# Kernel tuning notes

Hardware: AMD Instinct MI355X
Metric: run time of the kernel (lower is better)

## Reference

```python
import jax, jax.numpy as jnp
import numpy as np

B, S, D, E, H = 8, 1024, 1024, 8, 4096  # batch, seq, n_embd, num_experts, 4*n_embd


def setup_inputs() -> dict:
    key = jax.random.key(0)
    ks = jax.random.split(key, 8)
    sc = 0.02
    return {
        "x": jax.random.normal(ks[0], (B, S, D), jnp.float32),
        "noise": jax.random.normal(ks[1], (B, S, E), jnp.float32),
        "Wg": jax.random.normal(ks[2], (D, E), jnp.float32) * sc,
        "bg": jnp.zeros((E,), jnp.float32),
        "Wn": jax.random.normal(ks[3], (D, E), jnp.float32) * sc,
        "bn": jnp.zeros((E,), jnp.float32),
        "W1": jax.random.normal(ks[4], (E, D, H), jnp.float32) * sc,
        "b1": jnp.zeros((E, H), jnp.float32),
        "W2": jax.random.normal(ks[5], (E, H, D), jnp.float32) * sc,
        "b2": jnp.zeros((E, D), jnp.float32),
        "top_k": 2,
    }


def reference(x, noise, Wg, bg, Wn, bn, W1, b1, W2, b2, top_k):
    # --- NoisyTopkRouter ---
    logits = jnp.einsum("bsd,de->bse", x, Wg) + bg
    noise_logits = jnp.einsum("bsd,de->bse", x, Wn) + bn
    noisy = logits + noise * jax.nn.softplus(noise_logits)  # [B,S,E]
    _, idx = jax.lax.top_k(noisy, top_k)  # [B,S,K]
    in_topk = jax.nn.one_hot(idx, noisy.shape[-1], dtype=noisy.dtype).sum(-2) > 0
    sparse_logits = jnp.where(in_topk, noisy, -jnp.inf)
    gating = jax.nn.softmax(sparse_logits, axis=-1)  # zero outside top-k

    # --- dispatch/combine: gating is exactly zero for non-selected experts,
    # so per-expert masked gather + weighted scatter-add == gated dense sum ---
    g_e = jnp.moveaxis(gating, -1, 0)  # [E,B,S]

    def body(acc, params):
        W1e, b1e, W2e, b2e, ge = params
        h = jax.nn.relu(jnp.einsum("bsd,dh->bsh", x, W1e) + b1e)  # [B,S,H]
        y = (jnp.einsum("bsh,hd->bsd", h, W2e) + b2e) * ge[..., None]
        return acc + y, y

    final_output, expert_outputs = jax.lax.scan(
        body, jnp.zeros_like(x), (W1, b1, W2, b2, g_e)
    )
    # expert_outputs: [E,B,S,D], matching the per-expert weighted outputs list
    return final_output, expert_outputs, gating
```

## Files before the change

### kernel.cpp

```cpp
#include <hip/hip_runtime.h>
#include <hip/hip_bf16.h>
#include <stdint.h>

#define TKN   8192
#define DD    1024
#define EE    8
#define HH    4096
#define TOPK  2
#define NASG  (TKN * TOPK)
#define NSLOT 72

typedef unsigned short u16;
typedef __bf16 bf16x8 __attribute__((ext_vector_type(8)));
typedef float  f32x4  __attribute__((ext_vector_type(4)));

__device__ __forceinline__ u16 f2bf(float f) {
  __hip_bfloat16 h = __float2bfloat16(f);
  return __builtin_bit_cast(u16, h);
}
__device__ __forceinline__ float bf2f(u16 u) {
  uint32_t v = ((uint32_t)u) << 16;
  return __builtin_bit_cast(float, v);
}

__device__ __forceinline__ void glds16(const void* g, void* l) {
  __builtin_amdgcn_global_load_lds(
      (__attribute__((address_space(1))) void*)g,
      (__attribute__((address_space(3))) void*)l, 16, 0, 0);
}

#define FENCE() asm volatile("" ::: "memory")
#define BAR()   do { FENCE(); __builtin_amdgcn_s_barrier(); FENCE(); } while (0)
#define VMCNT0() asm volatile("s_waitcnt vmcnt(0)" ::: "memory")

__global__ __launch_bounds__(256) void transpose_cvt_kernel(
    const float* __restrict__ src, u16* __restrict__ dst, int R, int C) {
  __shared__ float tile[64][33];
  int e = blockIdx.z;
  int c0 = blockIdx.x * 32, r0 = blockIdx.y * 64;
  int tx = threadIdx.x, ty = threadIdx.y;
  const float* s = src + (size_t)e * R * C;
  uint32_t* d32 = (uint32_t*)(dst + (size_t)e * R * C);
#pragma unroll
  for (int j = 0; j < 8; j++)
    tile[ty * 8 + j][tx] = s[(size_t)(r0 + ty * 8 + j) * C + c0 + tx];
  __syncthreads();
#pragma unroll
  for (int jj = 0; jj < 4; jj++) {
    int c = c0 + ty * 4 + jj;
    uint32_t lo = f2bf(tile[2 * tx][ty * 4 + jj]);
    uint32_t hi = f2bf(tile[2 * tx + 1][ty * 4 + jj]);
    d32[((size_t)c * R + r0) / 2 + tx] = lo | (hi << 16);
  }
}

__global__ __launch_bounds__(256) void router_kernel(
    const float* __restrict__ x, const float* __restrict__ noise,
    const float* __restrict__ Wg, const float* __restrict__ bg,
    const float* __restrict__ Wn, const float* __restrict__ bn,
    float* __restrict__ gating, u16* __restrict__ xb,
    int* __restrict__ sel_e, float* __restrict__ sel_g) {
  int t = blockIdx.x;
  int tid = threadIdx.x;
  float acc[16];
#pragma unroll
  for (int j = 0; j < 16; j++) acc[j] = 0.f;
  for (int i = tid; i < DD; i += 256) {
    float xv = x[(size_t)t * DD + i];
    xb[(size_t)t * DD + i] = f2bf(xv);
    const float4* g4 = (const float4*)(Wg + (size_t)i * EE);
    const float4* n4 = (const float4*)(Wn + (size_t)i * EE);
    float4 ga = g4[0], gb = g4[1];
    float4 na = n4[0], nb = n4[1];
    acc[0] += xv * ga.x;  acc[1] += xv * ga.y;  acc[2] += xv * ga.z;  acc[3] += xv * ga.w;
    acc[4] += xv * gb.x;  acc[5] += xv * gb.y;  acc[6] += xv * gb.z;  acc[7] += xv * gb.w;
    acc[8] += xv * na.x;  acc[9] += xv * na.y;  acc[10] += xv * na.z; acc[11] += xv * na.w;
    acc[12] += xv * nb.x; acc[13] += xv * nb.y; acc[14] += xv * nb.z; acc[15] += xv * nb.w;
  }
  __shared__ float red[4][16];
  int lane = tid & 63, wv = tid >> 6;
#pragma unroll
  for (int j = 0; j < 16; j++) {
    float v = acc[j];
    for (int o = 32; o > 0; o >>= 1) v += __shfl_down(v, o);
    acc[j] = v;
  }
  if (lane == 0) {
#pragma unroll
    for (int j = 0; j < 16; j++) red[wv][j] = acc[j];
  }
  __syncthreads();
  if (tid == 0) {
    float nz[EE];
#pragma unroll
    for (int e = 0; e < EE; e++) {
      float dg = red[0][e] + red[1][e] + red[2][e] + red[3][e] + bg[e];
      float dn = red[0][8 + e] + red[1][8 + e] + red[2][8 + e] + red[3][8 + e] + bn[e];
      float sp = fmaxf(dn, 0.f) + log1pf(expf(-fabsf(dn)));
      nz[e] = dg + noise[(size_t)t * EE + e] * sp;
    }
    int m1 = 0;
    for (int e = 1; e < EE; e++) if (nz[e] > nz[m1]) m1 = e;
    int m2 = (m1 == 0) ? 1 : 0;
    for (int e = 0; e < EE; e++) if (e != m1 && nz[e] > nz[m2]) m2 = e;
    float eb = expf(nz[m2] - nz[m1]);
    float den = 1.f + eb;
    float g1 = 1.f / den, g2 = eb / den;
    gating[(size_t)t * EE + m1] = g1;
    gating[(size_t)t * EE + m2] = g2;
    sel_e[t * 2] = m1; sel_e[t * 2 + 1] = m2;
    sel_g[t * 2] = g1; sel_g[t * 2 + 1] = g2;
  }
}

__global__ __launch_bounds__(256) void hist_scan_kernel(
    const int* __restrict__ sel_e, int* __restrict__ counts,
    int* __restrict__ offsets, int* __restrict__ cursors,
    int* __restrict__ slots) {
  __shared__ int hist[EE];
  int tid = threadIdx.x;
  if (tid < EE) hist[tid] = 0;
  __syncthreads();
  for (int i = tid; i < NASG; i += 256) atomicAdd(&hist[sel_e[i]], 1);
  __syncthreads();
  if (tid == 0) {
    int off = 0, ns = 0;
    for (int e = 0; e < EE; e++) {
      int c = hist[e];
      counts[e] = c; offsets[e] = off; cursors[e] = off; off += c;
      int nrt = (c + 255) >> 8;
      for (int rt = 0; rt < nrt; rt++) slots[ns++] = (e << 16) | rt;
    }
    for (; ns < NSLOT; ns++) slots[ns] = -1;
  }
}

__global__ __launch_bounds__(256) void build_lists_kernel(
    const int* __restrict__ sel_e, const float* __restrict__ sel_g,
    int* __restrict__ cursors, int* __restrict__ tok_list,
    float* __restrict__ gate_list, int* __restrict__ asg_of) {
  int t = blockIdx.x * 256 + threadIdx.x;
  int lane = threadIdx.x & 63;
#pragma unroll
  for (int k = 0; k < TOPK; k++) {
    int e = sel_e[t * 2 + k];
    float g = sel_g[t * 2 + k];
    for (int ee = 0; ee < EE; ee++) {
      unsigned long long m = __ballot(e == ee);
      if (m) {
        int leader = __ffsll(m) - 1;
        int base = 0;
        if (lane == leader) base = atomicAdd(&cursors[ee], __popcll(m));
        base = __shfl(base, leader);
        if (e == ee) {
          int slot = base + __popcll(m & ((1ull << lane) - 1ull));
          tok_list[slot] = t;
          gate_list[slot] = g;
          asg_of[t * 2 + k] = slot;
        }
      }
    }
  }
}

__global__ __launch_bounds__(256) void zerofill_kernel(
    const float* __restrict__ gating, float* __restrict__ expert_out) {
  int id = blockIdx.x;
  int e = id >> 13, t = id & (TKN - 1);
  if (gating[(size_t)t * EE + e] != 0.f) return;
  float4* p = (float4*)(expert_out + ((size_t)e * TKN + t) * DD);
  p[threadIdx.x] = (float4){0.f, 0.f, 0.f, 0.f};
}

__global__ __launch_bounds__(256) void combine_kernel(
    const float* __restrict__ expert_out, const int* __restrict__ sel_e,
    float* __restrict__ final_out) {
  int t = blockIdx.x;
  int e1 = sel_e[2 * t], e2 = sel_e[2 * t + 1];
  const float4* r1 = (const float4*)(expert_out + ((size_t)e1 * TKN + t) * DD);
  const float4* r2 = (const float4*)(expert_out + ((size_t)e2 * TKN + t) * DD);
  float4* o = (float4*)(final_out + (size_t)t * DD);
  int i = threadIdx.x;
  float4 a = r1[i], b = r2[i];
  o[i] = (float4){a.x + b.x, a.y + b.y, a.z + b.z, a.w + b.w};
}

__global__ __launch_bounds__(256) void merge_combine_kernel(
    const u16* __restrict__ part, const int* __restrict__ asg_of,
    const int* __restrict__ sel_e, const float* __restrict__ sel_g,
    const float* __restrict__ b2, float* __restrict__ expert_out,
    float* __restrict__ final_out) {
  int t = blockIdx.x;
  int i = threadIdx.x;
  int i1 = asg_of[2 * t], i2 = asg_of[2 * t + 1];
  int e1 = sel_e[2 * t], e2 = sel_e[2 * t + 1];
  float g1 = sel_g[2 * t], g2 = sel_g[2 * t + 1];
  float s1[4] = {0.f, 0.f, 0.f, 0.f}, s2[4] = {0.f, 0.f, 0.f, 0.f};
#pragma unroll
  for (int kq = 0; kq < 4; kq++) {
    ushort4 a = ((const ushort4*)(part + ((size_t)kq * NASG + i1) * DD))[i];
    ushort4 b = ((const ushort4*)(part + ((size_t)kq * NASG + i2) * DD))[i];
    s1[0] += bf2f(a.x); s1[1] += bf2f(a.y); s1[2] += bf2f(a.z); s1[3] += bf2f(a.w);
    s2[0] += bf2f(b.x); s2[1] += bf2f(b.y); s2[2] += bf2f(b.z); s2[3] += bf2f(b.w);
  }
  float4 bb1 = ((const float4*)(b2 + (size_t)e1 * DD))[i];
  float4 bb2 = ((const float4*)(b2 + (size_t)e2 * DD))[i];
  float4 y1 = {(s1[0] + bb1.x) * g1, (s1[1] + bb1.y) * g1,
               (s1[2] + bb1.z) * g1, (s1[3] + bb1.w) * g1};
  float4 y2 = {(s2[0] + bb2.x) * g2, (s2[1] + bb2.y) * g2,
               (s2[2] + bb2.z) * g2, (s2[3] + bb2.w) * g2};
  ((float4*)(expert_out + ((size_t)e1 * TKN + t) * DD))[i] = y1;
  ((float4*)(expert_out + ((size_t)e2 * TKN + t) * DD))[i] = y2;
  ((float4*)(final_out + (size_t)t * DD))[i] =
      (float4){y1.x + y2.x, y1.y + y2.y, y1.z + y2.z, y1.w + y2.w};
}

template<int KLOOP, int KSTRIDE, bool GATHER, int EPI, int LOGC>
__global__ __launch_bounds__(512, 2) void gemm8_kernel(
    const u16* __restrict__ A, const u16* __restrict__ Bm,
    const float* __restrict__ bias, const int* __restrict__ tok_list,
    const float* __restrict__ gate_list, const int* __restrict__ counts,
    const int* __restrict__ offsets, const int* __restrict__ slots,
    int Ncols, u16* __restrict__ OutBf, float* __restrict__ outF,
    u16* __restrict__ outP) {
  constexpr int NT = KLOOP / 64;
  int gid = blockIdx.x;
  int q = gid >> 3;
  constexpr int PERX = 9 << LOGC;
  int kq = q / PERX;
  int r0q = q - kq * PERX;
  int slot = (gid & 7) * 9 + (r0q >> LOGC);
  int ct = r0q & ((1 << LOGC) - 1);
  int packed = slots[slot];
  if (packed < 0) return;
  int e = packed >> 16;
  int rt = packed & 0xffff;
  int cnt = counts[e];
  int off = offsets[e];
  int col0 = ct * 256;
  int k0e = kq * KLOOP;

  __shared__ __attribute__((aligned(16))) char ldsc[131072];

  int tid = threadIdx.x;
  int w = tid >> 6, l = tid & 63;
  int wm = w >> 2, wn = w & 3;
  int fr = l & 15, hi = l >> 4;
  int kk16 = hi << 4;
  int xr = (fr & 7) << 4;

  int rl0 = w * 8 + (l >> 3);
  int slotE = ((l & 7) ^ ((l >> 3) & 7)) << 3;
  const u16* aptr[4];
  const u16* bptr[4];
#pragma unroll
  for (int i = 0; i < 4; i++) {
    int r = rt * 256 + rl0 + i * 64;
    if (GATHER) {
      int idx = min(off + r, NASG - 1);
      aptr[i] = A + (size_t)tok_list[idx] * KSTRIDE + k0e + slotE;
    } else {
      aptr[i] = A + (size_t)(off + r) * KSTRIDE + k0e + slotE;
    }
    bptr[i] = Bm + ((size_t)e * Ncols + col0 + rl0 + i * 64) * KSTRIDE + k0e + slotE;
  }
  char* ldsA = ldsc;
  char* ldsB = ldsc + 65536;

  auto issueAB = [&](int t) {
    char* db = ldsB + (t & 1) * 32768 + w * 1024;
    char* da = ldsA + (t & 1) * 32768 + w * 1024;
    glds16(bptr[0] + t * 64, db);
    glds16(bptr[1] + t * 64, db + 8192);
    glds16(bptr[2] + t * 64, db + 16384);
    glds16(bptr[3] + t * 64, db + 24576);
    glds16(aptr[0] + t * 64, da);
    glds16(aptr[1] + t * 64, da + 8192);
    glds16(aptr[2] + t * 64, da + 16384);
    glds16(aptr[3] + t * 64, da + 24576);
  };

  f32x4 acc[8][4];
#pragma unroll
  for (int m = 0; m < 8; m++)
#pragma unroll
    for (int n = 0; n < 4; n++) acc[m][n] = (f32x4){0.f, 0.f, 0.f, 0.f};
  bf16x8 aF[4][2], bF0[2][2], bF1[2][2];

  issueAB(0);
  VMCNT0();
  BAR();

  for (int t = 0; t < NT; t++) {
    int abase = (t & 1) * 32768;
    int bbase = 65536 + (t & 1) * 32768;
    if (t + 1 < NT) issueAB(t + 1);
#pragma unroll
    for (int mm = 0; mm < 4; mm++)
#pragma unroll
      for (int ks = 0; ks < 2; ks++)
        aF[mm][ks] = *(const bf16x8*)(ldsc + abase + (wm * 128 + mm * 16 + fr) * 128 +
                                      ((ks * 64 + kk16) ^ xr));
#pragma unroll
    for (int nn = 0; nn < 2; nn++)
#pragma unroll
      for (int ks = 0; ks < 2; ks++) {
        bF0[nn][ks] = *(const bf16x8*)(ldsc + bbase + (wn * 64 + nn * 16 + fr) * 128 +
                                       ((ks * 64 + kk16) ^ xr));
        bF1[nn][ks] = *(const bf16x8*)(ldsc + bbase + (wn * 64 + 32 + nn * 16 + fr) * 128 +
                                       ((ks * 64 + kk16) ^ xr));
      }
    __builtin_amdgcn_s_setprio(1);
#pragma unroll
    for (int mm = 0; mm < 4; mm++) {
#pragma unroll
      for (int nn = 0; nn < 2; nn++)
#pragma unroll
        for (int ks = 0; ks < 2; ks++) {
          acc[mm][nn]     = __builtin_amdgcn_mfma_f32_16x16x32_bf16(aF[mm][ks], bF0[nn][ks], acc[mm][nn], 0, 0, 0);
          acc[mm][2 + nn] = __builtin_amdgcn_mfma_f32_16x16x32_bf16(aF[mm][ks], bF1[nn][ks], acc[mm][2 + nn], 0, 0, 0);
        }
      __builtin_amdgcn_sched_barrier(0);
#pragma unroll
      for (int ks = 0; ks < 2; ks++)
        aF[mm][ks] = *(const bf16x8*)(ldsc + abase + (wm * 128 + 64 + mm * 16 + fr) * 128 +
                                      ((ks * 64 + kk16) ^ xr));
      __builtin_amdgcn_sched_barrier(0);
    }
#pragma unroll
    for (int mm = 0; mm < 4; mm++)
#pragma unroll
      for (int nn = 0; nn < 2; nn++)
#pragma unroll
        for (int ks = 0; ks < 2; ks++) {
          acc[4 + mm][nn]     = __builtin_amdgcn_mfma_f32_16x16x32_bf16(aF[mm][ks], bF0[nn][ks], acc[4 + mm][nn], 0, 0, 0);
          acc[4 + mm][2 + nn] = __builtin_amdgcn_mfma_f32_16x16x32_bf16(aF[mm][ks], bF1[nn][ks], acc[4 + mm][2 + nn], 0, 0, 0);
        }
    __builtin_amdgcn_s_setprio(0);
    VMCNT0();
    BAR();
  }

  float biasN[4];
  int cN[4];
#pragma unroll
  for (int n = 0; n < 4; n++) {
    cN[n] = col0 + wn * 64 + (n >> 1) * 32 + (n & 1) * 16 + fr;
    biasN[n] = (EPI == 2) ? 0.f : bias[e * Ncols + cN[n]];
  }
  if constexpr (EPI == 0) {
#pragma unroll
    for (int m = 0; m < 8; m++) {
      int rb = rt * 256 + wm * 128 + (m >> 2) * 64 + (m & 3) * 16 + hi * 4;
#pragma unroll
      for (int j = 0; j < 4; j++) {
        int r = rb + j;
        if (r < cnt) {
#pragma unroll
          for (int n = 0; n < 4; n++) {
            float v = acc[m][n][j] + biasN[n];
            OutBf[(size_t)(off + r) * Ncols + cN[n]] = f2bf(fmaxf(v, 0.f));
          }
        }
      }
    }
  } else if constexpr (EPI == 1) {
#pragma unroll
    for (int m = 0; m < 8; m++) {
      int rb = rt * 256 + wm * 128 + (m >> 2) * 64 + (m & 3) * 16 + hi * 4;
#pragma unroll
      for (int j = 0; j < 4; j++) {
        int r = rb + j;
        if (r < cnt) {
          int idx = off + r;
          int tok = tok_list[idx];
          float g = gate_list[idx];
          size_t erow = ((size_t)e * TKN + tok) * DD;
#pragma unroll
          for (int n = 0; n < 4; n++)
            outF[erow + cN[n]] = (acc[m][n][j] + biasN[n]) * g;
        }
      }
    }
  } else {
#pragma unroll
    for (int m = 0; m < 8; m++) {
      int rb = rt * 256 + wm * 128 + (m >> 2) * 64 + (m & 3) * 16 + hi * 4;
#pragma unroll
      for (int j = 0; j < 4; j++) {
        int r = rb + j;
        if (r < cnt) {
          size_t prow = ((size_t)kq * NASG + off + r) * DD;
#pragma unroll
          for (int n = 0; n < 4; n++)
            outP[prow + cN[n]] = f2bf(acc[m][n][j]);
        }
      }
    }
  }
}

extern "C" void kernel_launch(void* const* d_in, const int* in_sizes, int n_in,
                              void* d_out, int out_size, void* d_ws, size_t ws_size,
                              hipStream_t stream) {
  const float* x     = (const float*)d_in[0];
  const float* noise = (const float*)d_in[1];
  const float* Wg    = (const float*)d_in[2];
  const float* bg    = (const float*)d_in[3];
  const float* Wn    = (const float*)d_in[4];
  const float* bn    = (const float*)d_in[5];
  const float* W1    = (const float*)d_in[6];
  const float* b1    = (const float*)d_in[7];
  const float* W2    = (const float*)d_in[8];
  const float* b2    = (const float*)d_in[9];

  float* final_out  = (float*)d_out;
  float* expert_out = final_out + (size_t)TKN * DD;
  float* gating     = expert_out + (size_t)EE * TKN * DD;

  char* ws = (char*)d_ws;
  size_t o = 0;
  auto alloc = [&](size_t bytes) {
    char* p = ws + o;
    o += bytes;
    o = (o + 255) & ~(size_t)255;
    return p;
  };
  u16*   xb        = (u16*)alloc((size_t)TKN * DD * 2);
  u16*   w1t       = (u16*)alloc((size_t)EE * HH * DD * 2);
  u16*   w2t       = (u16*)alloc((size_t)EE * DD * HH * 2);
  u16*   hbuf      = (u16*)alloc(((size_t)NASG + 256) * HH * 2);
  int*   tok_list  = (int*)alloc((size_t)NASG * 4);
  float* gate_list = (float*)alloc((size_t)NASG * 4);
  int*   sel_e     = (int*)alloc((size_t)NASG * 4);
  float* sel_g     = (float*)alloc((size_t)NASG * 4);
  int*   asg_of    = (int*)alloc((size_t)NASG * 4);
  int*   counts    = (int*)alloc(256);
  int*   offsets   = (int*)alloc(256);
  int*   cursors   = (int*)alloc(256);
  int*   slots     = (int*)alloc(NSLOT * 4);
  u16*   part      = (u16*)alloc((size_t)4 * NASG * DD * 2);
  bool use_split = (o <= ws_size);

  hipMemsetAsync(gating, 0, (size_t)TKN * EE * sizeof(float), stream);

  router_kernel<<<TKN, 256, 0, stream>>>(x, noise, Wg, bg, Wn, bn, gating, xb, sel_e, sel_g);
  hist_scan_kernel<<<1, 256, 0, stream>>>(sel_e, counts, offsets, cursors, slots);
  build_lists_kernel<<<TKN / 256, 256, 0, stream>>>(sel_e, sel_g, cursors, tok_list,
                                                    gate_list, asg_of);
  zerofill_kernel<<<EE * TKN, 256, 0, stream>>>(gating, expert_out);

  transpose_cvt_kernel<<<dim3(HH / 32, DD / 64, EE), dim3(32, 8), 0, stream>>>(W1, w1t, DD, HH);
  transpose_cvt_kernel<<<dim3(DD / 32, HH / 64, EE), dim3(32, 8), 0, stream>>>(W2, w2t, HH, DD);

  gemm8_kernel<DD, DD, true, 0, 4><<<8 * 9 * 16, 512, 0, stream>>>(
      xb, w1t, b1, tok_list, nullptr, counts, offsets, slots, HH, hbuf, nullptr, nullptr);

  if (use_split) {
    gemm8_kernel<HH / 4, HH, false, 2, 2><<<8 * 9 * 4 * 4, 512, 0, stream>>>(
        hbuf, w2t, b2, tok_list, gate_list, counts, offsets, slots, DD, nullptr, nullptr, part);
    merge_combine_kernel<<<TKN, 256, 0, stream>>>(part, asg_of, sel_e, sel_g, b2,
                                                  expert_out, final_out);
  } else {
    gemm8_kernel<HH, HH, false, 1, 2><<<8 * 9 * 4, 512, 0, stream>>>(
        hbuf, w2t, b2, tok_list, gate_list, counts, offsets, slots, DD, nullptr, expert_out, nullptr);
    combine_kernel<<<TKN, 256, 0, stream>>>(expert_out, sel_e, final_out);
  }
}
```

Measured before the change: 609.7 us.

## Shrink GEMM tiles to 128x256 with 256 threads and fold zero-fill into writers

The grouped expert GEMM moves from a 512-thread 256x256 tile with a K-step of 64 to a 256-thread 128x256 tile with a K-step of 32. Row tiles become 128 tokens, so the slot table grows, padding waste on ragged expert counts shrinks and the launch has more blocks. LDS use drops from 128KB to 48KB per block, which could allow more blocks per CU. The separate gating memset and expert_out zerofill kernel are dropped: the router writes all eight gating entries and the finalize kernel writes zeros for unselected experts. Each block now does less reuse per loaded byte, and the smaller K-step means twice as many barriers.

Result: no change. 619.9 us (+1.7%).

```diff
diff --git a/kernel.cpp b/kernel.cpp
--- a/kernel.cpp
+++ b/kernel.cpp
@@ -8,7 +8,8 @@
 #define HH    4096
 #define TOPK  2
 #define NASG  (TKN * TOPK)
-#define NSLOT 72
+#define NSLOT 136
+#define SLOTX 17
 
 typedef unsigned short u16;
 typedef __bf16 bf16x8 __attribute__((ext_vector_type(8)));
@@ -106,8 +107,9 @@
     float eb = expf(nz[m2] - nz[m1]);
     float den = 1.f + eb;
     float g1 = 1.f / den, g2 = eb / den;
-    gating[(size_t)t * EE + m1] = g1;
-    gating[(size_t)t * EE + m2] = g2;
+#pragma unroll
+    for (int e = 0; e < EE; e++)
+      gating[(size_t)t * EE + e] = (e == m1) ? g1 : (e == m2) ? g2 : 0.f;
     sel_e[t * 2] = m1; sel_e[t * 2 + 1] = m2;
     sel_g[t * 2] = g1; sel_g[t * 2 + 1] = g2;
   }
@@ -128,7 +130,7 @@
     for (int e = 0; e < EE; e++) {
       int c = hist[e];
       counts[e] = c; offsets[e] = off; cursors[e] = off; off += c;
-      int nrt = (c + 255) >> 8;
+      int nrt = (c + 127) >> 7;
       for (int rt = 0; rt < nrt; rt++) slots[ns++] = (e << 16) | rt;
     }
     for (; ns < NSLOT; ns++) slots[ns] = -1;
@@ -185,7 +187,7 @@
   o[i] = (float4){a.x + b.x, a.y + b.y, a.z + b.z, a.w + b.w};
 }
 
-__global__ __launch_bounds__(256) void merge_combine_kernel(
+__global__ __launch_bounds__(256) void finalize_kernel(
     const u16* __restrict__ part, const int* __restrict__ asg_of,
     const int* __restrict__ sel_e, const float* __restrict__ sel_g,
     const float* __restrict__ b2, float* __restrict__ expert_out,
@@ -209,27 +211,31 @@
                (s1[2] + bb1.z) * g1, (s1[3] + bb1.w) * g1};
   float4 y2 = {(s2[0] + bb2.x) * g2, (s2[1] + bb2.y) * g2,
                (s2[2] + bb2.z) * g2, (s2[3] + bb2.w) * g2};
-  ((float4*)(expert_out + ((size_t)e1 * TKN + t) * DD))[i] = y1;
-  ((float4*)(expert_out + ((size_t)e2 * TKN + t) * DD))[i] = y2;
+  float4 z = {0.f, 0.f, 0.f, 0.f};
+#pragma unroll
+  for (int e = 0; e < EE; e++) {
+    float4 v = (e == e1) ? y1 : (e == e2) ? y2 : z;
+    ((float4*)(expert_out + ((size_t)e * TKN + t) * DD))[i] = v;
+  }
   ((float4*)(final_out + (size_t)t * DD))[i] =
       (float4){y1.x + y2.x, y1.y + y2.y, y1.z + y2.z, y1.w + y2.w};
 }
 
 template<int KLOOP, int KSTRIDE, bool GATHER, int EPI, int LOGC>
-__global__ __launch_bounds__(512, 2) void gemm8_kernel(
+__global__ __launch_bounds__(256, 2) void gemm4_kernel(
     const u16* __restrict__ A, const u16* __restrict__ Bm,
     const float* __restrict__ bias, const int* __restrict__ tok_list,
     const float* __restrict__ gate_list, const int* __restrict__ counts,
     const int* __restrict__ offsets, const int* __restrict__ slots,
     int Ncols, u16* __restrict__ OutBf, float* __restrict__ outF,
     u16* __restrict__ outP) {
-  constexpr int NT = KLOOP / 64;
+  constexpr int NT = KLOOP / 32;
   int gid = blockIdx.x;
   int q = gid >> 3;
-  constexpr int PERX = 9 << LOGC;
+  constexpr int PERX = SLOTX << LOGC;
   int kq = q / PERX;
   int r0q = q - kq * PERX;
-  int slot = (gid & 7) * 9 + (r0q >> LOGC);
+  int slot = (gid & 7) * SLOTX + (r0q >> LOGC);
   int ct = r0q & ((1 << LOGC) - 1);
   int packed = slots[slot];
   if (packed < 0) return;
@@ -240,44 +246,42 @@
   int col0 = ct * 256;
   int k0e = kq * KLOOP;
 
-  __shared__ __attribute__((aligned(16))) char ldsc[131072];
+  __shared__ __attribute__((aligned(16))) char ldsc[49152];
 
   int tid = threadIdx.x;
   int w = tid >> 6, l = tid & 63;
-  int wm = w >> 2, wn = w & 3;
+  int wn = w;
   int fr = l & 15, hi = l >> 4;
-  int kk16 = hi << 4;
-  int xr = (fr & 7) << 4;
-
-  int rl0 = w * 8 + (l >> 3);
-  int slotE = ((l & 7) ^ ((l >> 3) & 7)) << 3;
-  const u16* aptr[4];
+  int koff = (hi ^ ((fr >> 1) & 3)) << 4;
+
+  int rowL = tid >> 2;
+  int gch = (tid & 3) ^ ((rowL >> 1) & 3);
+  const u16* aptr[2];
   const u16* bptr[4];
 #pragma unroll
-  for (int i = 0; i < 4; i++) {
-    int r = rt * 256 + rl0 + i * 64;
+  for (int i = 0; i < 2; i++) {
+    int r = rt * 128 + i * 64 + rowL;
     if (GATHER) {
       int idx = min(off + r, NASG - 1);
-      aptr[i] = A + (size_t)tok_list[idx] * KSTRIDE + k0e + slotE;
+      aptr[i] = A + (size_t)tok_list[idx] * KSTRIDE + k0e + gch * 8;
     } else {
-      aptr[i] = A + (size_t)(off + r) * KSTRIDE + k0e + slotE;
-    }
-    bptr[i] = Bm + ((size_t)e * Ncols + col0 + rl0 + i * 64) * KSTRIDE + k0e + slotE;
-  }
-  char* ldsA = ldsc;
-  char* ldsB = ldsc + 65536;
+      aptr[i] = A + (size_t)(off + r) * KSTRIDE + k0e + gch * 8;
+    }
+  }
+#pragma unroll
+  for (int i = 0; i < 4; i++)
+    bptr[i] = Bm + ((size_t)e * Ncols + col0 + i * 64 + rowL) * KSTRIDE + k0e + gch * 8;
 
   auto issueAB = [&](int t) {
-    char* db = ldsB + (t & 1) * 32768 + w * 1024;
-    char* da = ldsA + (t & 1) * 32768 + w * 1024;
-    glds16(bptr[0] + t * 64, db);
-    glds16(bptr[1] + t * 64, db + 8192);
-    glds16(bptr[2] + t * 64, db + 16384);
-    glds16(bptr[3] + t * 64, db + 24576);
-    glds16(aptr[0] + t * 64, da);
-    glds16(aptr[1] + t * 64, da + 8192);
-    glds16(aptr[2] + t * 64, da + 16384);
-    glds16(aptr[3] + t * 64, da + 24576);
+    char* base = ldsc + (t & 1) * 24576;
+    char* da = base + w * 1024;
+    glds16(aptr[0] + t * 32, da);
+    glds16(aptr[1] + t * 32, da + 4096);
+    char* db = base + 8192 + w * 1024;
+    glds16(bptr[0] + t * 32, db);
+    glds16(bptr[1] + t * 32, db + 4096);
+    glds16(bptr[2] + t * 32, db + 8192);
+    glds16(bptr[3] + t * 32, db + 12288);
   };
 
   f32x4 acc[8][4];
@@ -285,57 +289,28 @@
   for (int m = 0; m < 8; m++)
 #pragma unroll
     for (int n = 0; n < 4; n++) acc[m][n] = (f32x4){0.f, 0.f, 0.f, 0.f};
-  bf16x8 aF[4][2], bF0[2][2], bF1[2][2];
+  bf16x8 aF[8], bF[4];
 
   issueAB(0);
   VMCNT0();
   BAR();
 
   for (int t = 0; t < NT; t++) {
-    int abase = (t & 1) * 32768;
-    int bbase = 65536 + (t & 1) * 32768;
+    int ab = (t & 1) * 24576;
+    int bb = ab + 8192;
     if (t + 1 < NT) issueAB(t + 1);
 #pragma unroll
-    for (int mm = 0; mm < 4; mm++)
-#pragma unroll
-      for (int ks = 0; ks < 2; ks++)
-        aF[mm][ks] = *(const bf16x8*)(ldsc + abase + (wm * 128 + mm * 16 + fr) * 128 +
-                                      ((ks * 64 + kk16) ^ xr));
-#pragma unroll
-    for (int nn = 0; nn < 2; nn++)
-#pragma unroll
-      for (int ks = 0; ks < 2; ks++) {
-        bF0[nn][ks] = *(const bf16x8*)(ldsc + bbase + (wn * 64 + nn * 16 + fr) * 128 +
-                                       ((ks * 64 + kk16) ^ xr));
-        bF1[nn][ks] = *(const bf16x8*)(ldsc + bbase + (wn * 64 + 32 + nn * 16 + fr) * 128 +
-                                       ((ks * 64 + kk16) ^ xr));
-      }
+    for (int m = 0; m < 8; m++)
+      aF[m] = *(const bf16x8*)(ldsc + ab + (m * 16 + fr) * 64 + koff);
+#pragma unroll
+    for (int n = 0; n < 4; n++)
+      bF[n] = *(const bf16x8*)(ldsc + bb + (wn * 64 + n * 16 + fr) * 64 + koff);
     __builtin_amdgcn_s_setprio(1);
 #pragma unroll
-    for (int mm = 0; mm < 4; mm++) {
-#pragma unroll
-      for (int nn = 0; nn < 2; nn++)
-#pragma unroll
-        for (int ks = 0; ks < 2; ks++) {
-          acc[mm][nn]     = __builtin_amdgcn_mfma_f32_16x16x32_bf16(aF[mm][ks], bF0[nn][ks], acc[mm][nn], 0, 0, 0);
-          acc[mm][2 + nn] = __builtin_amdgcn_mfma_f32_16x16x32_bf16(aF[mm][ks], bF1[nn][ks], acc[mm][2 + nn], 0, 0, 0);
-        }
-      __builtin_amdgcn_sched_barrier(0);
-#pragma unroll
-      for (int ks = 0; ks < 2; ks++)
-        aF[mm][ks] = *(const bf16x8*)(ldsc + abase + (wm * 128 + 64 + mm * 16 + fr) * 128 +
-                                      ((ks * 64 + kk16) ^ xr));
-      __builtin_amdgcn_sched_barrier(0);
-    }
-#pragma unroll
-    for (int mm = 0; mm < 4; mm++)
-#pragma unroll
-      for (int nn = 0; nn < 2; nn++)
-#pragma unroll
-        for (int ks = 0; ks < 2; ks++) {
-          acc[4 + mm][nn]     = __builtin_amdgcn_mfma_f32_16x16x32_bf16(aF[mm][ks], bF0[nn][ks], acc[4 + mm][nn], 0, 0, 0);
-          acc[4 + mm][2 + nn] = __builtin_amdgcn_mfma_f32_16x16x32_bf16(aF[mm][ks], bF1[nn][ks], acc[4 + mm][2 + nn], 0, 0, 0);
-        }
+    for (int m = 0; m < 8; m++)
+#pragma unroll
+      for (int n = 0; n < 4; n++)
+        acc[m][n] = __builtin_amdgcn_mfma_f32_16x16x32_bf16(aF[m], bF[n], acc[m][n], 0, 0, 0);
     __builtin_amdgcn_s_setprio(0);
     VMCNT0();
     BAR();
@@ -345,13 +320,13 @@
   int cN[4];
 #pragma unroll
   for (int n = 0; n < 4; n++) {
-    cN[n] = col0 + wn * 64 + (n >> 1) * 32 + (n & 1) * 16 + fr;
+    cN[n] = col0 + wn * 64 + n * 16 + fr;
     biasN[n] = (EPI == 2) ? 0.f : bias[e * Ncols + cN[n]];
   }
   if constexpr (EPI == 0) {
 #pragma unroll
     for (int m = 0; m < 8; m++) {
-      int rb = rt * 256 + wm * 128 + (m >> 2) * 64 + (m & 3) * 16 + hi * 4;
+      int rb = rt * 128 + m * 16 + hi * 4;
 #pragma unroll
       for (int j = 0; j < 4; j++) {
         int r = rb + j;
@@ -367,7 +342,7 @@
   } else if constexpr (EPI == 1) {
 #pragma unroll
     for (int m = 0; m < 8; m++) {
-      int rb = rt * 256 + wm * 128 + (m >> 2) * 64 + (m & 3) * 16 + hi * 4;
+      int rb = rt * 128 + m * 16 + hi * 4;
 #pragma unroll
       for (int j = 0; j < 4; j++) {
         int r = rb + j;
@@ -385,7 +360,7 @@
   } else {
 #pragma unroll
     for (int m = 0; m < 8; m++) {
-      int rb = rt * 256 + wm * 128 + (m >> 2) * 64 + (m & 3) * 16 + hi * 4;
+      int rb = rt * 128 + m * 16 + hi * 4;
 #pragma unroll
       for (int j = 0; j < 4; j++) {
         int r = rb + j;
@@ -442,27 +417,25 @@
   u16*   part      = (u16*)alloc((size_t)4 * NASG * DD * 2);
   bool use_split = (o <= ws_size);
 
-  hipMemsetAsync(gating, 0, (size_t)TKN * EE * sizeof(float), stream);
-
   router_kernel<<<TKN, 256, 0, stream>>>(x, noise, Wg, bg, Wn, bn, gating, xb, sel_e, sel_g);
   hist_scan_kernel<<<1, 256, 0, stream>>>(sel_e, counts, offsets, cursors, slots);
   build_lists_kernel<<<TKN / 256, 256, 0, stream>>>(sel_e, sel_g, cursors, tok_list,
                                                     gate_list, asg_of);
-  zerofill_kernel<<<EE * TKN, 256, 0, stream>>>(gating, expert_out);
 
   transpose_cvt_kernel<<<dim3(HH / 32, DD / 64, EE), dim3(32, 8), 0, stream>>>(W1, w1t, DD, HH);
   transpose_cvt_kernel<<<dim3(DD / 32, HH / 64, EE), dim3(32, 8), 0, stream>>>(W2, w2t, HH, DD);
 
-  gemm8_kernel<DD, DD, true, 0, 4><<<8 * 9 * 16, 512, 0, stream>>>(
+  gemm4_kernel<DD, DD, true, 0, 4><<<8 * (SLOTX << 4), 256, 0, stream>>>(
       xb, w1t, b1, tok_list, nullptr, counts, offsets, slots, HH, hbuf, nullptr, nullptr);
 
   if (use_split) {
-    gemm8_kernel<HH / 4, HH, false, 2, 2><<<8 * 9 * 4 * 4, 512, 0, stream>>>(
+    gemm4_kernel<HH / 4, HH, false, 2, 2><<<8 * (SLOTX << 2) * 4, 256, 0, stream>>>(
         hbuf, w2t, b2, tok_list, gate_list, counts, offsets, slots, DD, nullptr, nullptr, part);
-    merge_combine_kernel<<<TKN, 256, 0, stream>>>(part, asg_of, sel_e, sel_g, b2,
-                                                  expert_out, final_out);
+    finalize_kernel<<<TKN, 256, 0, stream>>>(part, asg_of, sel_e, sel_g, b2,
+                                             expert_out, final_out);
   } else {
-    gemm8_kernel<HH, HH, false, 1, 2><<<8 * 9 * 4, 512, 0, stream>>>(
+    zerofill_kernel<<<EE * TKN, 256, 0, stream>>>(gating, expert_out);
+    gemm4_kernel<HH, HH, false, 1, 2><<<8 * (SLOTX << 2), 256, 0, stream>>>(
         hbuf, w2t, b2, tok_list, gate_list, counts, offsets, slots, DD, nullptr, expert_out, nullptr);
     combine_kernel<<<TKN, 256, 0, stream>>>(expert_out, sel_e, final_out);
   }
```
